# Performance work log

Measured on AMD Instinct MI355X. Metric: run time of the kernel, lower is better.

Reference implementation:

```python
import math
import jax, jax.numpy as jnp
import numpy as np

B, N, D = 4, 4096, 1024
H, DH = 16, 64  # D == H * DH


def setup_inputs() -> dict:
    key = jax.random.key(0)
    ks = jax.random.split(key, 7)
    s = 1.0 / math.sqrt(D)
    return {
        "tens": jax.random.normal(ks[0], (B, N, D), dtype=jnp.float32),
        "Wq": jax.random.normal(ks[1], (D, D), dtype=jnp.float32) * s,
        "bq": jax.random.normal(ks[2], (D,), dtype=jnp.float32) * 0.01,
        "Wk": jax.random.normal(ks[3], (D, D), dtype=jnp.float32) * s,
        "bk": jax.random.normal(ks[4], (D,), dtype=jnp.float32) * 0.01,
        "Wv": jax.random.normal(ks[5], (D, D), dtype=jnp.float32) * s,
        "bv": jax.random.normal(ks[6], (D,), dtype=jnp.float32) * 0.01,
    }


def reference(tens, Wq, bq, Wk, bk, Wv, bv):
    b, n, d = tens.shape
    # projections (torch Linear: x @ W^T + b)
    q = (tens @ Wq.T + bq).reshape(b, n, H, DH)  # [B,N,H,DH]
    k = (tens @ Wk.T + bk).reshape(b, n, H, DH)
    v = (tens @ Wv.T + bv).reshape(b, n, H, DH)
    scale = (1.0 / math.sqrt(DH)) / math.sqrt(n)
    # No softmax between QK^T and V => linear, reassociate as Q @ (K^T V)
    # to avoid the O(N^2) attention matrix; identical math.
    ktv = jnp.einsum("bnhd,bnhe->bhde", k, v)          # [B,H,DH,DH]
    out = jnp.einsum("bnhd,bhde->bnhe", q, ktv) * scale  # [B,N,H,DH]
    return out.reshape(b, n, d)
```

## Files before the change

kernel.cpp:

```cpp
#include <hip/hip_runtime.h>

typedef unsigned short ushort_t;
typedef __attribute__((ext_vector_type(8))) __bf16 bf16x8;
typedef __attribute__((ext_vector_type(8))) unsigned short ushort8;
typedef __attribute__((ext_vector_type(4))) unsigned short ushort4_t;
typedef __attribute__((ext_vector_type(4))) float floatx4;

__device__ inline unsigned short f2bf(float f) {
  union { float f; unsigned u; } x; x.f = f;
  return (unsigned short)((x.u + 0x7FFFu + ((x.u >> 16) & 1u)) >> 16);
}
__device__ inline float bf2f(unsigned short v) {
  union { unsigned u; float f; } x; x.u = (unsigned)v << 16;
  return x.f;
}

__global__ void cvt_tr(const float* __restrict__ tens, ushort_t* __restrict__ Xbf,
                       ushort_t* __restrict__ XT, float* __restrict__ s,
                       const float* __restrict__ Wk, ushort_t* __restrict__ Wkbf,
                       const float* __restrict__ Wv, ushort_t* __restrict__ Wvbf) {
  int t = threadIdx.x;
  if (blockIdx.z == 4) {
    int flat = blockIdx.x + 16 * blockIdx.y;
    const float* in; ushort_t* out;
    if (flat < 512) { in = Wk; out = Wkbf; } else { in = Wv; out = Wvbf; flat -= 512; }
    int i = (flat * 256 + t) * 8;
    const float4* p = (const float4*)(in + i);
    float4 x = p[0], y = p[1];
    ushort8 o;
    o[0] = f2bf(x.x); o[1] = f2bf(x.y); o[2] = f2bf(x.z); o[3] = f2bf(x.w);
    o[4] = f2bf(y.x); o[5] = f2bf(y.y); o[6] = f2bf(y.z); o[7] = f2bf(y.w);
    *(ushort8*)(out + i) = o;
    return;
  }
  int b = blockIdx.z;
  int d0 = blockIdx.x * 64;
  int n0 = blockIdx.y * 64;
  __shared__ ushort_t sT[64 * 72];
  int nl = t >> 2, c16 = (t & 3) * 16;
  const float* src = tens + ((long)b << 22) + (long)(n0 + nl) * 1024 + d0 + c16;
  ushort8 o0, o1;
#pragma unroll
  for (int j = 0; j < 2; ++j) {
    float4 v0 = *(const float4*)(src + j * 8);
    float4 v1 = *(const float4*)(src + j * 8 + 4);
    ushort8 o;
    o[0] = f2bf(v0.x); o[1] = f2bf(v0.y); o[2] = f2bf(v0.z); o[3] = f2bf(v0.w);
    o[4] = f2bf(v1.x); o[5] = f2bf(v1.y); o[6] = f2bf(v1.z); o[7] = f2bf(v1.w);
#pragma unroll
    for (int i = 0; i < 8; ++i) sT[(c16 + j * 8 + i) * 72 + nl] = o[i];
    if (j == 0) o0 = o; else o1 = o;
  }
  ushort_t* xdst = Xbf + ((long)b << 22) + (long)(n0 + nl) * 1024 + d0 + c16;
  *(ushort8*)xdst = o0;
  *(ushort8*)(xdst + 8) = o1;
  __syncthreads();
  int dl = t >> 2, n16 = (t & 3) * 16;
  ushort8 t0 = *(const ushort8*)(sT + dl * 72 + n16);
  ushort8 t1 = *(const ushort8*)(sT + dl * 72 + n16 + 8);
  ushort_t* dst = XT + ((long)b << 22) + (long)(d0 + dl) * 4096 + n0 + n16;
  *(ushort8*)dst = t0;
  *(ushort8*)(dst + 8) = t1;
  float ps = 0.f;
#pragma unroll
  for (int i = 0; i < 8; ++i) ps += bf2f(t0[i]) + bf2f(t1[i]);
  ps += __shfl_xor(ps, 1);
  ps += __shfl_xor(ps, 2);
  if ((t & 3) == 0) atomicAdd(&s[b * 1024 + d0 + dl], ps);
}

__device__ inline void gload_lds16(const void* g, void* l) {
  __builtin_amdgcn_global_load_lds(
      (const __attribute__((address_space(1))) unsigned int*)g,
      (__attribute__((address_space(3))) unsigned int*)l, 16, 0, 0);
}

__device__ inline void store_out(float* p, float v) { *p = v; }
__device__ inline void store_out(ushort_t* p, float v) { *p = f2bf(v); }

template <int K, bool BIAS, typename OutT>
__global__ void gemm_bt(const ushort_t* __restrict__ A, const ushort_t* __restrict__ Bm,
                        const float* __restrict__ bias, OutT* __restrict__ C,
                        int N, long sA_, long sB_, long sBias_, long sC_) {
  int gx = gridDim.x, gxy = gridDim.x * gridDim.y;
  int flat = blockIdx.x + gx * blockIdx.y + gxy * blockIdx.z;
  int total = gxy * gridDim.z;
  int per = total >> 3;
  int nf = (flat & 7) * per + (flat >> 3);
  int bz = nf / gxy; int rem = nf - bz * gxy;
  int by = rem / gx; int bx = rem - by * gx;

  A += (long)bz * sA_; Bm += (long)bz * sB_; C += (long)bz * sC_;
  if (BIAS) bias += (long)bz * sBias_;

  __shared__ ushort_t sA[2][128 * 32];
  __shared__ ushort_t sB[2][128 * 32];

  int t = threadIdx.x;
  int w = t >> 6, l = t & 63;
  int wy = w >> 1, wx = w & 1;
  int quad = l >> 4, m16 = l & 15;
  int mBase = by * 128, nBase = bx * 128;

  int r = l >> 2, pk = l & 3;
  int sCol = (pk ^ ((r >> 1) & 3)) * 8;
  int sRow0 = w * 32 + r;
  const ushort_t* gA0 = A + (long)(mBase + sRow0) * K + sCol;
  const ushort_t* gA1 = gA0 + 16 * K;
  const ushort_t* gB0 = Bm + (long)(nBase + sRow0) * K + sCol;
  const ushort_t* gB1 = gB0 + 16 * K;
  int lOff0 = (w * 2) * 512;
  int lOff1 = lOff0 + 512;

  int swzR = (m16 >> 1) & 3;
  int aOff = (wy * 64 + m16) * 32 + (quad ^ swzR) * 8;
  int bOff = (wx * 64 + m16) * 32 + (quad ^ swzR) * 8;

  floatx4 acc[4][4] = {};
  const int NS = K / 32;

  gload_lds16(gA0, sA[0] + lOff0);
  gload_lds16(gA1, sA[0] + lOff1);
  gload_lds16(gB0, sB[0] + lOff0);
  gload_lds16(gB1, sB[0] + lOff1);
  __syncthreads();

  for (int kt = 0; kt < NS; ++kt) {
    if (kt + 1 < NS) {
      int nb = (kt + 1) & 1, ko = (kt + 1) * 32;
      gload_lds16(gA0 + ko, sA[nb] + lOff0);
      gload_lds16(gA1 + ko, sA[nb] + lOff1);
      gload_lds16(gB0 + ko, sB[nb] + lOff0);
      gload_lds16(gB1 + ko, sB[nb] + lOff1);
    }
    __builtin_amdgcn_sched_barrier(0);
    const ushort_t* pa = sA[kt & 1];
    const ushort_t* pbm = sB[kt & 1];
    bf16x8 af[4], bfr[4];
#pragma unroll
    for (int i = 0; i < 4; ++i) af[i] = *(const bf16x8*)(pa + aOff + i * 16 * 32);
#pragma unroll
    for (int i = 0; i < 4; ++i) bfr[i] = *(const bf16x8*)(pbm + bOff + i * 16 * 32);
#pragma unroll
    for (int mi = 0; mi < 4; ++mi)
#pragma unroll
      for (int ni = 0; ni < 4; ++ni)
        acc[mi][ni] = __builtin_amdgcn_mfma_f32_16x16x32_bf16(af[mi], bfr[ni], acc[mi][ni], 0, 0, 0);
    if (kt + 1 < NS) __syncthreads();
  }

#pragma unroll
  for (int ni = 0; ni < 4; ++ni) {
    int n = nBase + wx * 64 + ni * 16 + m16;
    float bb = 0.f;
    if (BIAS) bb = bias[n];
#pragma unroll
    for (int mi = 0; mi < 4; ++mi) {
      int m0 = mBase + wy * 64 + mi * 16 + quad * 4;
      floatx4 v = acc[mi][ni];
#pragma unroll
      for (int rr = 0; rr < 4; ++rr)
        store_out(&C[(long)(m0 + rr) * N + n], v[rr] + bb);
    }
  }
}

template <int K, bool SYM, typename OutT>
__global__ void gemm64(const ushort_t* __restrict__ A, const ushort_t* __restrict__ Bm,
                       OutT* __restrict__ C, int N, long sA_, long sB_, long sC_) {
  int bz, byy, bxx;
  if (SYM) {
    int flat = blockIdx.x + gridDim.x * blockIdx.y;
    int per = (gridDim.x * gridDim.y) >> 3;
    int nf = (flat & 7) * per + (flat >> 3);
    bz = nf / 136;
    int tri = nf - bz * 136;
    byy = (int)((__fsqrt_rn(8.0f * tri + 1.0f) - 1.0f) * 0.5f);
    while ((byy + 1) * (byy + 2) / 2 <= tri) ++byy;
    while (byy * (byy + 1) / 2 > tri) --byy;
    bxx = tri - byy * (byy + 1) / 2;
  } else {
    int gx = gridDim.x, gxy = gridDim.x * gridDim.y;
    int flat = blockIdx.x + gx * blockIdx.y + gxy * blockIdx.z;
    int total = gxy * gridDim.z;
    int per = total >> 3;
    int nf = (flat & 7) * per + (flat >> 3);
    bz = nf / gxy; int rem = nf - bz * gxy;
    byy = rem / gx; bxx = rem - byy * gx;
  }

  A += (long)bz * sA_; Bm += (long)bz * sB_; C += (long)bz * sC_;

  __shared__ ushort_t sA[2][2][64 * 32];
  __shared__ ushort_t sB[2][2][64 * 32];

  int t = threadIdx.x;
  int w = t >> 6, l = t & 63;
  int wy = w >> 1, wx = w & 1;
  int quad = l >> 4, m16 = l & 15;
  int mBase = byy * 64, nBase = bxx * 64;

  int r = l >> 2, pk = l & 3;
  int sCol = (pk ^ ((r >> 1) & 3)) * 8;
  int sRow = w * 16 + r;
  const ushort_t* gA = A + (long)(mBase + sRow) * K + sCol;
  const ushort_t* gB = Bm + (long)(nBase + sRow) * K + sCol;
  int lOff = w * 512;

  int swzR = (m16 >> 1) & 3;
  int aOff = (wy * 32 + m16) * 32 + (quad ^ swzR) * 8;
  int bOff = (wx * 32 + m16) * 32 + (quad ^ swzR) * 8;

  floatx4 acc[2][2] = {};
  const int NS = K / 64;

#pragma unroll
  for (int kk = 0; kk < 2; ++kk) {
    gload_lds16(gA + kk * 32, sA[0][kk] + lOff);
    gload_lds16(gB + kk * 32, sB[0][kk] + lOff);
  }
  __syncthreads();

  for (int kt = 0; kt < NS; ++kt) {
    if (kt + 1 < NS) {
      int nb = (kt + 1) & 1, ko = (kt + 1) * 64;
#pragma unroll
      for (int kk = 0; kk < 2; ++kk) {
        gload_lds16(gA + ko + kk * 32, sA[nb][kk] + lOff);
        gload_lds16(gB + ko + kk * 32, sB[nb][kk] + lOff);
      }
    }
    __builtin_amdgcn_sched_barrier(0);
    int cb = kt & 1;
    bf16x8 af[2][2], bfr[2][2];
#pragma unroll
    for (int kk = 0; kk < 2; ++kk) {
#pragma unroll
      for (int i = 0; i < 2; ++i) {
        af[i][kk] = *(const bf16x8*)(sA[cb][kk] + aOff + i * 16 * 32);
        bfr[i][kk] = *(const bf16x8*)(sB[cb][kk] + bOff + i * 16 * 32);
      }
    }
#pragma unroll
    for (int kk = 0; kk < 2; ++kk)
#pragma unroll
      for (int mi = 0; mi < 2; ++mi)
#pragma unroll
        for (int ni = 0; ni < 2; ++ni)
          acc[mi][ni] = __builtin_amdgcn_mfma_f32_16x16x32_bf16(af[mi][kk], bfr[ni][kk], acc[mi][ni], 0, 0, 0);
    if (kt + 1 < NS) __syncthreads();
  }

#pragma unroll
  for (int ni = 0; ni < 2; ++ni) {
    int n = nBase + wx * 32 + ni * 16 + m16;
#pragma unroll
    for (int mi = 0; mi < 2; ++mi) {
      int m0 = mBase + wy * 32 + mi * 16 + quad * 4;
      floatx4 v = acc[mi][ni];
#pragma unroll
      for (int rr = 0; rr < 4; ++rr)
        store_out(&C[(long)(m0 + rr) * N + n], v[rr]);
      if (SYM) {
        if (byy != bxx) {
          ushort4_t pkv;
#pragma unroll
          for (int rr = 0; rr < 4; ++rr) pkv[rr] = f2bf(v[rr]);
          *(ushort4_t*)((ushort_t*)C + (long)n * N + m0) = pkv;
        }
      }
    }
  }
}

__global__ void uw_kernel(const ushort_t* __restrict__ Wkbf, const ushort_t* __restrict__ Wvbf,
                          const float* __restrict__ s, float* __restrict__ u,
                          float* __restrict__ wv_s) {
  int id = blockIdx.x;
  int b = id & 3, which = (id >> 2) & 1, chunk = id >> 3;
  const ushort_t* W = which ? Wvbf : Wkbf;
  float* o = which ? wv_s : u;
  __shared__ float ss[1024];
  int t = threadIdx.x;
  *(float4*)(ss + t * 4) = *(const float4*)(s + b * 1024 + t * 4);
  __syncthreads();
  int r = chunk * 256 + t;
  const ushort_t* row = W + (long)r * 1024;
  float acc = 0.f;
  for (int k = 0; k < 1024; k += 8) {
    ushort8 v = *(const ushort8*)(row + k);
#pragma unroll
    for (int i = 0; i < 8; ++i) acc += bf2f(v[i]) * ss[k + i];
  }
  o[b * 1024 + r] = acc;
}

__global__ void make_w2(const ushort_t* __restrict__ T1, const ushort_t* __restrict__ Wvbf,
                        const float* __restrict__ u, const float* __restrict__ wv_s,
                        const float* __restrict__ bk, const float* __restrict__ bv,
                        const float* __restrict__ Wq, const float* __restrict__ bq,
                        ushort_t* __restrict__ W2T, float* __restrict__ bias2, float scale) {
  int bh = blockIdx.x, cq = blockIdx.y;
  int b = bh >> 4, h = bh & 15;
  __shared__ float sKTV[64 * 64];
  __shared__ float sW[64 * 64];
  int t = threadIdx.x, w = t >> 6, l = t & 63;
  int quad = l >> 4, m16 = l & 15;

  const ushort_t* Arow = T1 + ((long)b << 20) + (long)(h * 64 + w * 16 + m16) * 1024 + quad * 8;
  const ushort_t* Brow = Wvbf + (long)(h * 64 + m16) * 1024 + quad * 8;
  floatx4 acc[4] = {};
  for (int kt = 0; kt < 1024; kt += 32) {
    bf16x8 af = *(const bf16x8*)(Arow + kt);
#pragma unroll
    for (int j = 0; j < 4; ++j) {
      bf16x8 bfv = *(const bf16x8*)(Brow + (long)j * 16 * 1024 + kt);
      acc[j] = __builtin_amdgcn_mfma_f32_16x16x32_bf16(af, bfv, acc[j], 0, 0, 0);
    }
  }
#pragma unroll
  for (int j = 0; j < 4; ++j) {
    int e = j * 16 + m16;
    float bve = bv[h * 64 + e];
    float wse = wv_s[b * 1024 + h * 64 + e] + 4096.f * bve;
#pragma unroll
    for (int rr = 0; rr < 4; ++rr) {
      int d = w * 16 + quad * 4 + rr;
      float corr = u[b * 1024 + h * 64 + d] * bve + bk[h * 64 + d] * wse;
      sKTV[d * 64 + e] = acc[j][rr] + corr;
    }
  }
  __syncthreads();

  if (cq == 0 && t < 64) {
    float s = 0.f;
    for (int d = 0; d < 64; ++d) s += bq[h * 64 + d] * sKTV[d * 64 + t];
    bias2[b * 1024 + h * 64 + t] = s * scale;
  }

  int e = t >> 2, c0 = (t & 3) * 16;
  for (int ct = cq * 256; ct < cq * 256 + 256; ct += 64) {
    __syncthreads();
    {
      int d = t >> 2, cc = (t & 3) * 16;
#pragma unroll
      for (int j = 0; j < 16; j += 4)
        *(float4*)(sW + d * 64 + cc + j) =
            *(const float4*)(Wq + (long)(h * 64 + d) * 1024 + ct + cc + j);
    }
    __syncthreads();
    float outv[16] = {};
    for (int d = 0; d < 64; ++d) {
      float kv = sKTV[d * 64 + e];
#pragma unroll
      for (int j = 0; j < 16; ++j) outv[j] += sW[d * 64 + c0 + j] * kv;
    }
    ushort8 o0, o1;
#pragma unroll
    for (int j = 0; j < 8; ++j) { o0[j] = f2bf(outv[j] * scale); o1[j] = f2bf(outv[8 + j] * scale); }
    ushort_t* dst = W2T + ((long)(b * 1024 + h * 64 + e)) * 1024 + ct + c0;
    *(ushort8*)dst = o0;
    *(ushort8*)(dst + 8) = o1;
  }
}

extern "C" void kernel_launch(void* const* d_in, const int* in_sizes, int n_in,
                              void* d_out, int out_size, void* d_ws, size_t ws_size,
                              hipStream_t stream) {
  (void)in_sizes; (void)n_in; (void)out_size; (void)ws_size;
  const float* tens = (const float*)d_in[0];
  const float* Wq = (const float*)d_in[1];
  const float* bq = (const float*)d_in[2];
  const float* Wk = (const float*)d_in[3];
  const float* bk = (const float*)d_in[4];
  const float* Wv = (const float*)d_in[5];
  const float* bv = (const float*)d_in[6];
  float* out = (float*)d_out;

  char* w = (char*)d_ws;
  ushort_t* Xbf  = (ushort_t*)(w);
  ushort_t* XT   = (ushort_t*)(w + 33554432);
  ushort_t* Wkbf = (ushort_t*)(w + 67108864);
  ushort_t* Wvbf = (ushort_t*)(w + 69206016);
  ushort_t* Gbf  = (ushort_t*)(w + 71303168);
  ushort_t* T1   = (ushort_t*)(w + 79691776);
  float*    s    = (float*)(w + 88080384);
  float*    u    = (float*)(w + 88096768);
  float*    wv_s = (float*)(w + 88113152);
  ushort_t* W2T  = (ushort_t*)(w + 89178112);
  float*    bias2= (float*)(w + 97566720);

  const float scale = (1.0f / 8.0f) / 64.0f;

  hipMemsetAsync(s, 0, 16384, stream);
  hipLaunchKernelGGL(cvt_tr, dim3(16, 64, 5), dim3(256), 0, stream,
                     tens, Xbf, XT, s, Wk, Wkbf, Wv, Wvbf);

  hipLaunchKernelGGL((gemm64<4096, true, ushort_t>), dim3(136, 4, 1), dim3(256), 0, stream,
                     XT, XT, Gbf, 1024, 4194304L, 4194304L, 1048576L);

  hipLaunchKernelGGL(uw_kernel, dim3(32), dim3(256), 0, stream, Wkbf, Wvbf, s, u, wv_s);

  hipLaunchKernelGGL((gemm64<1024, false, ushort_t>), dim3(16, 16, 4), dim3(256), 0, stream,
                     Wkbf, Gbf, T1, 1024, 0L, 1048576L, 1048576L);

  hipLaunchKernelGGL(make_w2, dim3(64, 4), dim3(256), 0, stream,
                     T1, Wvbf, u, wv_s, bk, bv, Wq, bq, W2T, bias2, scale);

  hipLaunchKernelGGL((gemm_bt<1024, true, float>), dim3(8, 32, 4), dim3(256), 0, stream,
                     Xbf, W2T, bias2, out, 1024,
                     4194304L, 1048576L, 1024L, 4194304L);
}
```

Before: 293.2 us.

## Replace syncthreads with vmcnt waits, deepen Gram K-tile, drop atomics

Inside the GEMM main loops, the block-wide syncthreads around async global-to-LDS loads are replaced with explicit s_waitcnt vmcnt counts plus raw barriers, so prefetches for the next tile can stay in flight while the current tile is consumed. The Gram GEMM over K=4096 now stages four 32-wide K slices per iteration instead of two, halving the number of barrier rounds at the cost of more LDS. The column-sum atomics and the memset are replaced by per-block partial sums that uw_kernel reduces. The hand-counted vmcnt values must match the number of outstanding loads exactly, otherwise stale LDS data could be read.

Measured after the change: 310.5 us. 1.06x slower.

```diff
diff --git a/kernel.cpp b/kernel.cpp
--- a/kernel.cpp
+++ b/kernel.cpp
@@ -15,8 +15,17 @@
   return x.f;
 }
 
+__device__ inline void bar() {
+  asm volatile("" ::: "memory");
+  __builtin_amdgcn_s_barrier();
+  asm volatile("" ::: "memory");
+}
+#define WAITV4 asm volatile("s_waitcnt vmcnt(4)" ::: "memory")
+#define WAITV8 asm volatile("s_waitcnt vmcnt(8)" ::: "memory")
+#define WAITV0 asm volatile("s_waitcnt vmcnt(0)" ::: "memory")
+
 __global__ void cvt_tr(const float* __restrict__ tens, ushort_t* __restrict__ Xbf,
-                       ushort_t* __restrict__ XT, float* __restrict__ s,
+                       ushort_t* __restrict__ XT, float* __restrict__ spart,
                        const float* __restrict__ Wk, ushort_t* __restrict__ Wkbf,
                        const float* __restrict__ Wv, ushort_t* __restrict__ Wvbf) {
   int t = threadIdx.x;
@@ -66,7 +75,7 @@
   for (int i = 0; i < 8; ++i) ps += bf2f(t0[i]) + bf2f(t1[i]);
   ps += __shfl_xor(ps, 1);
   ps += __shfl_xor(ps, 2);
-  if ((t & 3) == 0) atomicAdd(&s[b * 1024 + d0 + dl], ps);
+  if ((t & 3) == 0) spart[(((long)b << 6) + blockIdx.y) * 1024 + d0 + dl] = ps;
 }
 
 __device__ inline void gload_lds16(const void* g, void* l) {
@@ -123,7 +132,6 @@
   gload_lds16(gA1, sA[0] + lOff1);
   gload_lds16(gB0, sB[0] + lOff0);
   gload_lds16(gB1, sB[0] + lOff1);
-  __syncthreads();
 
   for (int kt = 0; kt < NS; ++kt) {
     if (kt + 1 < NS) {
@@ -132,8 +140,11 @@
       gload_lds16(gA1 + ko, sA[nb] + lOff1);
       gload_lds16(gB0 + ko, sB[nb] + lOff0);
       gload_lds16(gB1 + ko, sB[nb] + lOff1);
-    }
-    __builtin_amdgcn_sched_barrier(0);
+      WAITV4;
+    } else {
+      WAITV0;
+    }
+    bar();
     const ushort_t* pa = sA[kt & 1];
     const ushort_t* pbm = sB[kt & 1];
     bf16x8 af[4], bfr[4];
@@ -146,7 +157,7 @@
 #pragma unroll
       for (int ni = 0; ni < 4; ++ni)
         acc[mi][ni] = __builtin_amdgcn_mfma_f32_16x16x32_bf16(af[mi], bfr[ni], acc[mi][ni], 0, 0, 0);
-    if (kt + 1 < NS) __syncthreads();
+    bar();
   }
 
 #pragma unroll
@@ -165,7 +176,7 @@
   }
 }
 
-template <int K, bool SYM, typename OutT>
+template <int K, int BKP, bool SYM, typename OutT>
 __global__ void gemm64(const ushort_t* __restrict__ A, const ushort_t* __restrict__ Bm,
                        OutT* __restrict__ C, int N, long sA_, long sB_, long sC_) {
   int bz, byy, bxx;
@@ -191,8 +202,8 @@
 
   A += (long)bz * sA_; Bm += (long)bz * sB_; C += (long)bz * sC_;
 
-  __shared__ ushort_t sA[2][2][64 * 32];
-  __shared__ ushort_t sB[2][2][64 * 32];
+  __shared__ ushort_t sA[2][BKP][64 * 32];
+  __shared__ ushort_t sB[2][BKP][64 * 32];
 
   int t = threadIdx.x;
   int w = t >> 6, l = t & 63;
@@ -212,43 +223,40 @@
   int bOff = (wx * 32 + m16) * 32 + (quad ^ swzR) * 8;
 
   floatx4 acc[2][2] = {};
-  const int NS = K / 64;
-
-#pragma unroll
-  for (int kk = 0; kk < 2; ++kk) {
+  const int NS = K / (32 * BKP);
+
+#pragma unroll
+  for (int kk = 0; kk < BKP; ++kk) {
     gload_lds16(gA + kk * 32, sA[0][kk] + lOff);
     gload_lds16(gB + kk * 32, sB[0][kk] + lOff);
   }
-  __syncthreads();
 
   for (int kt = 0; kt < NS; ++kt) {
     if (kt + 1 < NS) {
-      int nb = (kt + 1) & 1, ko = (kt + 1) * 64;
-#pragma unroll
-      for (int kk = 0; kk < 2; ++kk) {
+      int nb = (kt + 1) & 1, ko = (kt + 1) * 32 * BKP;
+#pragma unroll
+      for (int kk = 0; kk < BKP; ++kk) {
         gload_lds16(gA + ko + kk * 32, sA[nb][kk] + lOff);
         gload_lds16(gB + ko + kk * 32, sB[nb][kk] + lOff);
       }
-    }
-    __builtin_amdgcn_sched_barrier(0);
+      if constexpr (BKP == 2) { WAITV4; } else { WAITV8; }
+    } else {
+      WAITV0;
+    }
+    bar();
     int cb = kt & 1;
-    bf16x8 af[2][2], bfr[2][2];
-#pragma unroll
-    for (int kk = 0; kk < 2; ++kk) {
-#pragma unroll
-      for (int i = 0; i < 2; ++i) {
-        af[i][kk] = *(const bf16x8*)(sA[cb][kk] + aOff + i * 16 * 32);
-        bfr[i][kk] = *(const bf16x8*)(sB[cb][kk] + bOff + i * 16 * 32);
-      }
-    }
-#pragma unroll
-    for (int kk = 0; kk < 2; ++kk)
-#pragma unroll
-      for (int mi = 0; mi < 2; ++mi)
-#pragma unroll
-        for (int ni = 0; ni < 2; ++ni)
-          acc[mi][ni] = __builtin_amdgcn_mfma_f32_16x16x32_bf16(af[mi][kk], bfr[ni][kk], acc[mi][ni], 0, 0, 0);
-    if (kt + 1 < NS) __syncthreads();
+#pragma unroll
+    for (int kk = 0; kk < BKP; ++kk) {
+      bf16x8 af0 = *(const bf16x8*)(sA[cb][kk] + aOff);
+      bf16x8 af1 = *(const bf16x8*)(sA[cb][kk] + aOff + 16 * 32);
+      bf16x8 bf0 = *(const bf16x8*)(sB[cb][kk] + bOff);
+      bf16x8 bf1 = *(const bf16x8*)(sB[cb][kk] + bOff + 16 * 32);
+      acc[0][0] = __builtin_amdgcn_mfma_f32_16x16x32_bf16(af0, bf0, acc[0][0], 0, 0, 0);
+      acc[0][1] = __builtin_amdgcn_mfma_f32_16x16x32_bf16(af0, bf1, acc[0][1], 0, 0, 0);
+      acc[1][0] = __builtin_amdgcn_mfma_f32_16x16x32_bf16(af1, bf0, acc[1][0], 0, 0, 0);
+      acc[1][1] = __builtin_amdgcn_mfma_f32_16x16x32_bf16(af1, bf1, acc[1][1], 0, 0, 0);
+    }
+    bar();
   }
 
 #pragma unroll
@@ -274,7 +282,7 @@
 }
 
 __global__ void uw_kernel(const ushort_t* __restrict__ Wkbf, const ushort_t* __restrict__ Wvbf,
-                          const float* __restrict__ s, float* __restrict__ u,
+                          const float* __restrict__ spart, float* __restrict__ u,
                           float* __restrict__ wv_s) {
   int id = blockIdx.x;
   int b = id & 3, which = (id >> 2) & 1, chunk = id >> 3;
@@ -282,17 +290,23 @@
   float* o = which ? wv_s : u;
   __shared__ float ss[1024];
   int t = threadIdx.x;
-  *(float4*)(ss + t * 4) = *(const float4*)(s + b * 1024 + t * 4);
+  float4 a4 = {0.f, 0.f, 0.f, 0.f};
+  const float* sp = spart + ((long)b << 16) + t * 4;
+  for (int n0 = 0; n0 < 64; ++n0) {
+    float4 v = *(const float4*)(sp + n0 * 1024);
+    a4.x += v.x; a4.y += v.y; a4.z += v.z; a4.w += v.w;
+  }
+  *(float4*)(ss + t * 4) = a4;
   __syncthreads();
-  int r = chunk * 256 + t;
-  const ushort_t* row = W + (long)r * 1024;
+  int rr = chunk * 256 + t;
+  const ushort_t* row = W + (long)rr * 1024;
   float acc = 0.f;
   for (int k = 0; k < 1024; k += 8) {
     ushort8 v = *(const ushort8*)(row + k);
 #pragma unroll
     for (int i = 0; i < 8; ++i) acc += bf2f(v[i]) * ss[k + i];
   }
-  o[b * 1024 + r] = acc;
+  o[b * 1024 + rr] = acc;
 }
 
 __global__ void make_w2(const ushort_t* __restrict__ T1, const ushort_t* __restrict__ Wvbf,
@@ -384,24 +398,23 @@
   ushort_t* Wvbf = (ushort_t*)(w + 69206016);
   ushort_t* Gbf  = (ushort_t*)(w + 71303168);
   ushort_t* T1   = (ushort_t*)(w + 79691776);
-  float*    s    = (float*)(w + 88080384);
-  float*    u    = (float*)(w + 88096768);
-  float*    wv_s = (float*)(w + 88113152);
+  float*    spart= (float*)(w + 88080384);
+  float*    u    = (float*)(w + 89128960);
+  float*    wv_s = (float*)(w + 89145344);
   ushort_t* W2T  = (ushort_t*)(w + 89178112);
   float*    bias2= (float*)(w + 97566720);
 
   const float scale = (1.0f / 8.0f) / 64.0f;
 
-  hipMemsetAsync(s, 0, 16384, stream);
   hipLaunchKernelGGL(cvt_tr, dim3(16, 64, 5), dim3(256), 0, stream,
-                     tens, Xbf, XT, s, Wk, Wkbf, Wv, Wvbf);
-
-  hipLaunchKernelGGL((gemm64<4096, true, ushort_t>), dim3(136, 4, 1), dim3(256), 0, stream,
+                     tens, Xbf, XT, spart, Wk, Wkbf, Wv, Wvbf);
+
+  hipLaunchKernelGGL((gemm64<4096, 4, true, ushort_t>), dim3(136, 4, 1), dim3(256), 0, stream,
                      XT, XT, Gbf, 1024, 4194304L, 4194304L, 1048576L);
 
-  hipLaunchKernelGGL(uw_kernel, dim3(32), dim3(256), 0, stream, Wkbf, Wvbf, s, u, wv_s);
-
-  hipLaunchKernelGGL((gemm64<1024, false, ushort_t>), dim3(16, 16, 4), dim3(256), 0, stream,
+  hipLaunchKernelGGL(uw_kernel, dim3(32), dim3(256), 0, stream, Wkbf, Wvbf, spart, u, wv_s);
+
+  hipLaunchKernelGGL((gemm64<1024, 2, false, ushort_t>), dim3(16, 16, 4), dim3(256), 0, stream,
                      Wkbf, Gbf, T1, 1024, 0L, 1048576L, 1048576L);
 
   hipLaunchKernelGGL(make_w2, dim3(64, 4), dim3(256), 0, stream,
```
